# Optimization experiments

Hardware: AMD Instinct MI355X
Metric: run time of the kernel (lower is better)

Reference implementation:

```python
import jax, jax.numpy as jnp
import numpy as np

NUM_HEADS = 16


def setup_inputs() -> dict:
    key = jax.random.key(0)
    ks = jax.random.split(key, 7)
    B, Lq, Lkv, C, Lpos = 4, 1024, 2048, 1024, 1024
    s = 0.02
    return {
        "q": jax.random.normal(ks[0], (B, Lq, C), jnp.float32),
        "kv": jax.random.normal(ks[1], (B, Lkv, C), jnp.float32),
        "attn_pos": jax.random.normal(ks[2], (B, NUM_HEADS, Lq, Lpos), jnp.float32),
        "q_w": jax.random.normal(ks[3], (C, C), jnp.float32) * s,
        "kv_w": jax.random.normal(ks[4], (2 * C, C), jnp.float32) * s,
        "proj_w": jax.random.normal(ks[5], (C, C), jnp.float32) * s,
        "proj_b": jnp.zeros((C,), jnp.float32),
    }


def reference(q, kv, attn_pos, q_w, kv_w, proj_w, proj_b):
    B, Lq, C = q.shape
    Lkv = kv.shape[1]
    H = NUM_HEADS
    D = C // H
    scale = D ** (-0.5)

    # q projection -> (B, H, Lq, D)
    qh = (q @ q_w.T).reshape(B, Lq, H, D).transpose(0, 2, 1, 3)
    # kv projection -> k, v each (B, H, Lkv, D); torch Linear weight rows: first C -> k, next C -> v
    kvp = kv @ kv_w.T  # (B, Lkv, 2C)
    k = kvp[..., :C].reshape(B, Lkv, H, D).transpose(0, 2, 1, 3)
    v = kvp[..., C:].reshape(B, Lkv, H, D).transpose(0, 2, 1, 3)

    attn = jnp.einsum("bhqd,bhkd->bhqk", qh, k) * scale  # (B, H, Lq, Lkv)
    # zero-pad attn_pos on last dim to Lkv (matches torch cat-with-zeros)
    pad = Lkv - attn_pos.shape[-1]
    if pad > 0:
        attn_pos = jnp.pad(attn_pos, ((0, 0), (0, 0), (0, 0), (0, pad)))
    attn = jax.nn.softmax(attn + attn_pos, axis=-1)

    x = jnp.einsum("bhqk,bhkd->bhqd", attn, v)  # (B, H, Lq, D)
    x = x.transpose(0, 2, 1, 3).reshape(B, Lq, C)
    return x @ proj_w.T + proj_b
```

## Files before the change

kernel.cpp:

```cpp
#include <hip/hip_runtime.h>

using half_t = _Float16;
using half8  = __attribute__((ext_vector_type(8))) _Float16;
using half4  = __attribute__((ext_vector_type(4))) _Float16;
using half2v = __attribute__((ext_vector_type(2))) _Float16;
using f32x4  = __attribute__((ext_vector_type(4))) float;
using f32x16 = __attribute__((ext_vector_type(16))) float;

#define MFMA(a, b, c)   __builtin_amdgcn_mfma_f32_16x16x32_f16((a), (b), (c), 0, 0, 0)
#define MFMA32(a, b, c) __builtin_amdgcn_mfma_f32_32x32x16_f16((a), (b), (c), 0, 0, 0)

#define GLL16(g, l)                                                     \
  __builtin_amdgcn_global_load_lds(                                     \
      (__attribute__((address_space(1))) void*)(g),                     \
      (__attribute__((address_space(3))) void*)(l), 16, 0, 0)

__device__ __forceinline__ half8 ld8(const half_t* p) { return *(const half8*)p; }

__global__ void cvt_f32_f16(const float* __restrict__ src, half_t* __restrict__ dst, int n4) {
  int i = blockIdx.x * blockDim.x + threadIdx.x;
  if (i < n4) {
    f32x4 v = ((const f32x4*)src)[i];
    half4 h;
    h[0] = (half_t)v[0]; h[1] = (half_t)v[1]; h[2] = (half_t)v[2]; h[3] = (half_t)v[3];
    ((half4*)dst)[i] = h;
  }
}

template <int EPI>
__global__ __launch_bounds__(256) void gemm_kernel(
    const half_t* __restrict__ A, const half_t* __restrict__ Bt,
    int M, int N, int K,
    half_t* __restrict__ oh, half_t* __restrict__ ov,
    float* __restrict__ of, const float* __restrict__ bias) {
  __shared__ alignas(16) half_t sA[128 * 32];
  __shared__ alignas(16) half_t sB[128 * 32];
  const int tid  = threadIdx.x;
  const int lane = tid & 63;
  const int w    = tid >> 6;
  const int c    = lane & 15;
  const int quad = lane >> 4;
  const int m0 = blockIdx.y * 128;
  const int n0 = blockIdx.x * 128;
  const int wm = (w & 1) * 64;
  const int wn = (w >> 1) * 64;

  f32x4 acc[4][4] = {};

  const int srow = tid >> 2;
  const int scol = (tid & 3) * 8;
  const half_t* Ag = A + (size_t)(m0 + srow) * K + scol;
  const half_t* Bg = Bt + (size_t)(n0 + srow) * K + scol;

  for (int k0 = 0; k0 < K; k0 += 32) {
    GLL16(Ag + k0,            sA + tid * 8);
    GLL16(Ag + k0 + 64 * K,   sA + tid * 8 + 2048);
    GLL16(Bg + k0,            sB + tid * 8);
    GLL16(Bg + k0 + 64 * K,   sB + tid * 8 + 2048);
    __syncthreads();
    half8 a[4], b[4];
#pragma unroll
    for (int i = 0; i < 4; ++i) a[i] = ld8(&sA[(wm + i * 16 + c) * 32 + quad * 8]);
#pragma unroll
    for (int j = 0; j < 4; ++j) b[j] = ld8(&sB[(wn + j * 16 + c) * 32 + quad * 8]);
#pragma unroll
    for (int i = 0; i < 4; ++i)
#pragma unroll
      for (int j = 0; j < 4; ++j) acc[i][j] = MFMA(a[i], b[j], acc[i][j]);
    __syncthreads();
  }

#pragma unroll
  for (int i = 0; i < 4; ++i) {
    const int mbase = m0 + wm + i * 16 + quad * 4;
#pragma unroll
    for (int j = 0; j < 4; ++j) {
      const int n = n0 + wn + j * 16 + c;
      if (EPI == 0) {
        const int bb = mbase >> 10, qi = mbase & 1023;
        const int hh = n >> 6, d = n & 63;
        half_t* p = oh + (((size_t)(bb * 16 + hh) * 1024 + qi) * 64 + d);
#pragma unroll
        for (int r = 0; r < 4; ++r) p[(size_t)r * 64] = (half_t)acc[i][j][r];
      } else if (EPI == 1) {
        const int bb = mbase >> 11, kvi = mbase & 2047;
        if (n < 1024) {
          const int hh = n >> 6, d = n & 63;
          half_t* p = oh + (((size_t)(bb * 16 + hh) * 2048 + kvi) * 64 + d);
#pragma unroll
          for (int r = 0; r < 4; ++r) p[(size_t)r * 64] = (half_t)acc[i][j][r];
        } else {
          const int nn = n - 1024;
          const int hh = nn >> 6, d = nn & 63;
          half4 hv;
#pragma unroll
          for (int r = 0; r < 4; ++r) hv[r] = (half_t)acc[i][j][r];
          *(half4*)&ov[((size_t)(bb * 16 + hh) * 64 + d) * 2048 + kvi] = hv;
        }
      } else {
        const float bv = bias[n];
#pragma unroll
        for (int r = 0; r < 4; ++r) of[(size_t)(mbase + r) * N + n] = acc[i][j][r] + bv;
      }
    }
  }
}

__global__ __launch_bounds__(256, 2) void attn_kernel(
    const half_t* __restrict__ qh, const half_t* __restrict__ kk,
    const half_t* __restrict__ vt, const float* __restrict__ pos,
    half_t* __restrict__ xout) {
  __shared__ alignas(16) unsigned char smem[2][24576];

  const int tid  = threadIdx.x;
  const int lane = tid & 63;
  const int w    = tid >> 6;
  const int lr   = lane & 31;
  const int hi   = lane >> 5;

  const int bh  = blockIdx.x >> 3;
  const int q0b = (blockIdx.x & 7) * 128;
  const int q0w = q0b + w * 32;

  const char* kgb = (const char*)(kk + (size_t)bh * 2048 * 64);
  const char* vgb = (const char*)(vt + (size_t)bh * 64 * 2048);
  const char* pgb = (const char*)(pos + ((size_t)bh * 1024 + q0b) * 1024);

  const int krow = tid >> 3;
  const int kcsw = ((tid & 7) * 16) ^ ((krow & 7) << 4);
  const int vrow = tid >> 2;
  const int vcsw = ((tid & 3) * 16) ^ ((vrow & 3) << 4);

  half8 qf[4];
  {
    const half_t* qg = qh + ((size_t)bh * 1024 + q0w + lr) * 64 + hi * 8;
#pragma unroll
    for (int ks = 0; ks < 4; ++ks) qf[ks] = ld8(qg + ks * 16);
  }

  f32x16 oa0 = {}, oa1 = {};
  float m_run = -1e30f, l_run = 0.f;

  const float LOG2E = 1.4426950408889634f;
  const float SCL2E = 0.125f * 1.4426950408889634f;
  const int   kswz  = (lr & 7) << 4;
  const int   vswz  = (lr & 3) << 4;

  auto stage = [&](int buf, int kv0) {
    unsigned char* s = smem[buf];
    GLL16(kgb + (size_t)(kv0 + krow) * 128 + kcsw, s + tid * 16);
    GLL16(vgb + (size_t)vrow * 4096 + (size_t)kv0 * 2 + vcsw, s + 4096 + tid * 16);
    if (kv0 < 1024) {
#pragma unroll
      for (int i = 0; i < 4; ++i) {
        const int off  = (i * 256 + tid) * 16;
        const int prow = off >> 7;
        const int pc   = (off & 127) ^ ((prow & 7) << 4);
        GLL16(pgb + (size_t)prow * 4096 + (size_t)kv0 * 4 + pc, s + 8192 + off);
      }
    }
  };

  stage(0, 0);
  __syncthreads();

  for (int kv0 = 0; kv0 < 2048; kv0 += 32) {
    const int cur = (kv0 >> 5) & 1;
    const unsigned char* sb = smem[cur];
    if (kv0 + 32 < 2048) stage(cur ^ 1, kv0 + 32);

    f32x16 sreg = {};
#pragma unroll
    for (int ks = 0; ks < 4; ++ks) {
      const half8 kf = *(const half8*)(sb + lr * 128 + ((ks * 32 + hi * 16) ^ kswz));
      sreg = MFMA32(kf, qf[ks], sreg);
    }

    float lg[16];
    if (kv0 < 1024) {
      const unsigned char* sp = sb + 8192 + (size_t)(w * 32 + lr) * 128;
#pragma unroll
      for (int t = 0; t < 4; ++t) {
        const f32x4 pv = *(const f32x4*)(sp + ((t * 32 + hi * 16) ^ kswz));
#pragma unroll
        for (int u = 0; u < 4; ++u) lg[t * 4 + u] = sreg[t * 4 + u] * SCL2E + pv[u] * LOG2E;
      }
    } else {
#pragma unroll
      for (int r = 0; r < 16; ++r) lg[r] = sreg[r] * SCL2E;
    }

    float mx = lg[0];
#pragma unroll
    for (int r = 1; r < 16; ++r) mx = fmaxf(mx, lg[r]);
    mx = fmaxf(mx, __shfl_xor(mx, 32));
    if (__any(mx > m_run)) {
      const float mnew  = fmaxf(m_run, mx);
      const float alpha = exp2f(m_run - mnew);
#pragma unroll
      for (int r = 0; r < 16; ++r) { oa0[r] *= alpha; oa1[r] *= alpha; }
      l_run *= alpha;
      m_run = mnew;
    }
    float pe[16];
    float rs = 0.f;
#pragma unroll
    for (int r = 0; r < 16; ++r) { pe[r] = exp2f(lg[r] - m_run); rs += pe[r]; }
    rs += __shfl_xor(rs, 32);
    l_run += rs;

    unsigned int pk[8], xp[8];
#pragma unroll
    for (int e = 0; e < 8; ++e) {
      union { half2v h; unsigned int u; } cv;
      cv.h[0] = (half_t)pe[2 * e];
      cv.h[1] = (half_t)pe[2 * e + 1];
      pk[e] = cv.u;
    }
#pragma unroll
    for (int e = 0; e < 8; ++e) xp[e] = (unsigned int)__shfl_xor((int)pk[e], 32);

    union { unsigned int u[4]; half8 h; } bf0, bf1;
    if (hi) {
      bf0.u[0] = xp[2]; bf0.u[1] = xp[3]; bf0.u[2] = pk[2]; bf0.u[3] = pk[3];
      bf1.u[0] = xp[6]; bf1.u[1] = xp[7]; bf1.u[2] = pk[6]; bf1.u[3] = pk[7];
    } else {
      bf0.u[0] = pk[0]; bf0.u[1] = pk[1]; bf0.u[2] = xp[0]; bf0.u[3] = xp[1];
      bf1.u[0] = pk[4]; bf1.u[1] = pk[5]; bf1.u[2] = xp[4]; bf1.u[3] = xp[5];
    }

#pragma unroll
    for (int m = 0; m < 2; ++m) {
      const int co = (m * 32 + hi * 16) ^ vswz;
      const half8 vf0 = *(const half8*)(sb + 4096 + lr * 64 + co);
      const half8 vf1 = *(const half8*)(sb + 4096 + (32 + lr) * 64 + co);
      const half8 pb  = m ? bf1.h : bf0.h;
      oa0 = MFMA32(vf0, pb, oa0);
      oa1 = MFMA32(vf1, pb, oa1);
    }

    __syncthreads();
  }

  const float inv = 1.0f / l_run;
  half_t* xg = xout + ((size_t)(bh >> 4) * 1024 + q0w + lr) * 1024 + (bh & 15) * 64;
#pragma unroll
  for (int t = 0; t < 4; ++t) {
    half4 h0, h1;
#pragma unroll
    for (int u = 0; u < 4; ++u) {
      h0[u] = (half_t)(oa0[t * 4 + u] * inv);
      h1[u] = (half_t)(oa1[t * 4 + u] * inv);
    }
    *(half4*)(xg + t * 8 + hi * 4)      = h0;
    *(half4*)(xg + 32 + t * 8 + hi * 4) = h1;
  }
}

extern "C" void kernel_launch(void* const* d_in, const int* in_sizes, int n_in,
                              void* d_out, int out_size, void* d_ws, size_t ws_size,
                              hipStream_t stream) {
  const float* q   = (const float*)d_in[0];
  const float* kv  = (const float*)d_in[1];
  const float* pos = (const float*)d_in[2];
  const float* qw  = (const float*)d_in[3];
  const float* kvw = (const float*)d_in[4];
  const float* pw  = (const float*)d_in[5];
  const float* pb  = (const float*)d_in[6];
  float* out = (float*)d_out;

  char* ws = (char*)d_ws;
  half_t* qf   = (half_t*)(ws);
  half_t* kvf  = (half_t*)(ws + (size_t)(8)  * 1048576);
  half_t* qwf  = (half_t*)(ws + (size_t)(24) * 1048576);
  half_t* kvwf = (half_t*)(ws + (size_t)(26) * 1048576);
  half_t* pwf  = (half_t*)(ws + (size_t)(30) * 1048576);
  half_t* qh   = (half_t*)(ws + (size_t)(32) * 1048576);
  half_t* kk   = (half_t*)(ws + (size_t)(40) * 1048576);
  half_t* vt   = (half_t*)(ws + (size_t)(56) * 1048576);
  half_t* xb   = (half_t*)(ws + (size_t)(72) * 1048576);

  auto cvt = [&](const float* s, half_t* d, int n) {
    cvt_f32_f16<<<n / 1024, 256, 0, stream>>>(s, d, n / 4);
  };
  cvt(q,   qf,   4 * 1024 * 1024);
  cvt(kv,  kvf,  4 * 2048 * 1024);
  cvt(qw,  qwf,  1024 * 1024);
  cvt(kvw, kvwf, 2048 * 1024);
  cvt(pw,  pwf,  1024 * 1024);

  gemm_kernel<0><<<dim3(1024 / 128, 4096 / 128), 256, 0, stream>>>(
      qf, qwf, 4096, 1024, 1024, qh, nullptr, nullptr, nullptr);
  gemm_kernel<1><<<dim3(2048 / 128, 8192 / 128), 256, 0, stream>>>(
      kvf, kvwf, 8192, 2048, 1024, kk, vt, nullptr, nullptr);
  attn_kernel<<<4 * 16 * 8, 256, 0, stream>>>(qh, kk, vt, pos, xb);
  gemm_kernel<2><<<dim3(1024 / 128, 4096 / 128), 256, 0, stream>>>(
      xb, pwf, 4096, 1024, 1024, nullptr, nullptr, out, pb);
}
```

Baseline: 602.7 us.

## Triple-buffer attention K/V/pos staging with vmcnt-based waits and single barrier

Moves the attention kernel from double to triple buffering in LDS, so loads run two tiles ahead. Explicit s_waitcnt vmcnt counts plus a single barrier replace the per-iteration __syncthreads, and the loop is split into a pos-bearing phase and a pos-free phase because they issue different numbers of loads per stage. The V tile layout is also changed to 128-byte rows using the same XOR swizzle as K. The aim is to hide global-to-LDS latency, at the cost of 72KB of LDS per block, which may reduce occupancy under launch_bounds(256,2).

```diff
diff --git a/kernel.cpp b/kernel.cpp
--- a/kernel.cpp
+++ b/kernel.cpp
@@ -14,6 +14,8 @@
   __builtin_amdgcn_global_load_lds(                                     \
       (__attribute__((address_space(1))) void*)(g),                     \
       (__attribute__((address_space(3))) void*)(l), 16, 0, 0)
+
+#define WAITBAR(n) asm volatile("s_waitcnt vmcnt(" #n ")\n\ts_barrier" ::: "memory")
 
 __device__ __forceinline__ half8 ld8(const half_t* p) { return *(const half8*)p; }
 
@@ -110,7 +112,7 @@
     const half_t* __restrict__ qh, const half_t* __restrict__ kk,
     const half_t* __restrict__ vt, const float* __restrict__ pos,
     half_t* __restrict__ xout) {
-  __shared__ alignas(16) unsigned char smem[2][24576];
+  __shared__ alignas(16) unsigned char smem[3][24576];
 
   const int tid  = threadIdx.x;
   const int lane = tid & 63;
@@ -128,8 +130,9 @@
 
   const int krow = tid >> 3;
   const int kcsw = ((tid & 7) * 16) ^ ((krow & 7) << 4);
-  const int vrow = tid >> 2;
-  const int vcsw = ((tid & 3) * 16) ^ ((vrow & 3) << 4);
+  const int vrow = tid >> 3;
+  const int vlc  = ((tid & 7) * 16) ^ ((vrow & 7) << 4);
+  const char* vsrc = vgb + (size_t)(vrow + ((vlc >> 6) << 5)) * 4096 + (vlc & 63);
 
   half8 qf[4];
   {
@@ -137,6 +140,7 @@
 #pragma unroll
     for (int ks = 0; ks < 4; ++ks) qf[ks] = ld8(qg + ks * 16);
   }
+  asm volatile("s_waitcnt vmcnt(0)" ::: "memory");
 
   f32x16 oa0 = {}, oa1 = {};
   float m_run = -1e30f, l_run = 0.f;
@@ -144,12 +148,11 @@
   const float LOG2E = 1.4426950408889634f;
   const float SCL2E = 0.125f * 1.4426950408889634f;
   const int   kswz  = (lr & 7) << 4;
-  const int   vswz  = (lr & 3) << 4;
 
   auto stage = [&](int buf, int kv0) {
     unsigned char* s = smem[buf];
     GLL16(kgb + (size_t)(kv0 + krow) * 128 + kcsw, s + tid * 16);
-    GLL16(vgb + (size_t)vrow * 4096 + (size_t)kv0 * 2 + vcsw, s + 4096 + tid * 16);
+    GLL16(vsrc + (size_t)kv0 * 2, s + 4096 + tid * 16);
     if (kv0 < 1024) {
 #pragma unroll
       for (int i = 0; i < 4; ++i) {
@@ -161,14 +164,7 @@
     }
   };
 
-  stage(0, 0);
-  __syncthreads();
-
-  for (int kv0 = 0; kv0 < 2048; kv0 += 32) {
-    const int cur = (kv0 >> 5) & 1;
-    const unsigned char* sb = smem[cur];
-    if (kv0 + 32 < 2048) stage(cur ^ 1, kv0 + 32);
-
+  auto compute = [&](const unsigned char* sb, int kv0) {
     f32x16 sreg = {};
 #pragma unroll
     for (int ks = 0; ks < 4; ++ks) {
@@ -229,18 +225,32 @@
       bf1.u[0] = pk[4]; bf1.u[1] = pk[5]; bf1.u[2] = xp[4]; bf1.u[3] = xp[5];
     }
 
+    const unsigned char* sv = sb + 4096 + lr * 128;
 #pragma unroll
     for (int m = 0; m < 2; ++m) {
-      const int co = (m * 32 + hi * 16) ^ vswz;
-      const half8 vf0 = *(const half8*)(sb + 4096 + lr * 64 + co);
-      const half8 vf1 = *(const half8*)(sb + 4096 + (32 + lr) * 64 + co);
+      const half8 vf0 = *(const half8*)(sv + ((m * 32 + hi * 16) ^ kswz));
+      const half8 vf1 = *(const half8*)(sv + ((64 + m * 32 + hi * 16) ^ kswz));
       const half8 pb  = m ? bf1.h : bf0.h;
       oa0 = MFMA32(vf0, pb, oa0);
       oa1 = MFMA32(vf1, pb, oa1);
     }
-
-    __syncthreads();
-  }
+  };
+
+  stage(0, 0);
+  stage(1, 32);
+  int kv0 = 0;
+  for (int k = 0; k < 31; ++k, kv0 += 32) {
+    WAITBAR(6);
+    stage((k + 2) % 3, kv0 + 64);
+    compute(smem[k % 3], kv0);
+  }
+  for (int k = 31; k < 63; ++k, kv0 += 32) {
+    WAITBAR(2);
+    if (k < 62) stage((k + 2) % 3, kv0 + 64);
+    compute(smem[k % 3], kv0);
+  }
+  WAITBAR(0);
+  compute(smem[0], kv0);
 
   const float inv = 1.0f / l_run;
   half_t* xg = xout + ((size_t)(bh >> 4) * 1024 + q0w + lr) * 1024 + (bh & 15) * 64;
```

Result: no change. 591.2 us (-1.9%).
